# Kernel optimization log

Hardware: AMD Instinct MI355X
Metric: run time of the kernel (lower is better)

Reference implementation:

```python
import jax, jax.numpy as jnp
import numpy as np

DIM = 256
HEADS = 8
DIM_HEAD = 64
SLICE_NUM = 64
INNER = HEADS * DIM_HEAD  # 512
SCALE = DIM_HEAD ** -0.5


def setup_inputs() -> dict:
    key = jax.random.key(0)
    ks = jax.random.split(key, 12)
    b, n = 4, 32768
    s = 0.02
    inp = {
        "x": jax.random.normal(ks[0], (b, n, DIM), dtype=jnp.float32),
        # weights stored as [in, out] so y = x @ W + b
        "W_fx": jax.random.normal(ks[1], (DIM, INNER), dtype=jnp.float32) * s,
        "b_fx": jnp.zeros((INNER,), dtype=jnp.float32),
        "W_x": jax.random.normal(ks[2], (DIM, INNER), dtype=jnp.float32) * s,
        "b_x": jnp.zeros((INNER,), dtype=jnp.float32),
        "W_slice": jax.random.normal(ks[3], (DIM_HEAD, SLICE_NUM), dtype=jnp.float32) * s,
        "b_slice": jnp.zeros((SLICE_NUM,), dtype=jnp.float32),
        "temperature": jnp.ones((1, HEADS, 1, 1), dtype=jnp.float32) * 0.5,
        "Wq": jax.random.normal(ks[4], (DIM_HEAD, DIM_HEAD), dtype=jnp.float32) * s,
        "Wk": jax.random.normal(ks[5], (DIM_HEAD, DIM_HEAD), dtype=jnp.float32) * s,
        "Wv": jax.random.normal(ks[6], (DIM_HEAD, DIM_HEAD), dtype=jnp.float32) * s,
        "W_out": jax.random.normal(ks[7], (INNER, DIM), dtype=jnp.float32) * s,
        "b_out": jnp.zeros((DIM,), dtype=jnp.float32),
    }
    return inp


def reference(x, W_fx, b_fx, W_x, b_x, W_slice, b_slice, temperature,
              Wq, Wk, Wv, W_out, b_out):
    b, n, c = x.shape
    h, d, g = HEADS, DIM_HEAD, SLICE_NUM
    # input projections -> b h n d
    fx_mid = (x @ W_fx + b_fx).reshape(b, n, h, d).transpose(0, 2, 1, 3)
    x_mid = (x @ W_x + b_x).reshape(b, n, h, d).transpose(0, 2, 1, 3)
    # temperature-scaled slice routing softmax: b h n g
    temp = jnp.clip(temperature, 0.1, 5.0)
    slice_logits = (x_mid @ W_slice + b_slice) / temp
    slice_weights = jax.nn.softmax(slice_logits, axis=-1)
    # weighted pooling into slice tokens: b h g d
    slice_tokens = jnp.einsum('bhnc,bhng->bhgc', fx_mid, slice_weights)
    norm = jnp.sum(slice_weights, axis=2)  # b h g
    slice_tokens = slice_tokens / (norm[..., None] + 1e-5)
    # small attention over slice tokens
    q = slice_tokens @ Wq
    k = slice_tokens @ Wk
    v = slice_tokens @ Wv
    attn = jax.nn.softmax(jnp.einsum('bhgd,bhkd->bhgk', q, k) * SCALE, axis=-1)
    out_slice = jnp.einsum('bhgk,bhkd->bhgd', attn, v)
    # scatter back to points: b h n d -> b n (h d)
    out = jnp.einsum('bhgd,bhng->bhnd', out_slice, slice_weights)
    out = out.transpose(0, 2, 1, 3).reshape(b, n, h * d)
    return out @ W_out + b_out
```

## Files before the change

### kernel.cpp

```cpp
#include <hip/hip_runtime.h>
#include <hip/hip_bf16.h>
#include <stdint.h>

#define DIM 256
#define HEADS 8
#define INNER 512
#define NPTS 32768
#define PADN 136
#define PADD 72

typedef unsigned int uint32;
typedef short bf16x8 __attribute__((ext_vector_type(8)));
typedef float f32x4 __attribute__((ext_vector_type(4)));

static __device__ __forceinline__ unsigned short f2bf(float f) {
    unsigned int u = __float_as_uint(f);
    u += 0x7fffu + ((u >> 16) & 1u);
    return (unsigned short)(u >> 16);
}
static __device__ __forceinline__ float bf2f(unsigned short v) {
    return __uint_as_float(((unsigned int)v) << 16);
}
static __device__ __forceinline__ uint32 pkbf(float a, float b) {
    __hip_bfloat162 h = __float22bfloat162_rn(make_float2(a, b));
    return *(reinterpret_cast<uint32*>(&h));
}
static __device__ __forceinline__ void gll16(const void* g, const void* l) {
    __builtin_amdgcn_global_load_lds(
        (const __attribute__((address_space(1))) uint32*)g,
        (__attribute__((address_space(3))) uint32*)l, 16, 0, 0);
}

__global__ __launch_bounds__(256) void k_prep(
    const float* __restrict__ Wfx, const float* __restrict__ Wx,
    const float* __restrict__ Wsl, const float* __restrict__ x,
    unsigned short* __restrict__ Wbt, unsigned short* __restrict__ WslT,
    unsigned short* __restrict__ xb)
{
    const int blk = blockIdx.x, t = threadIdx.x;
    if (blk < 4) {
        const int n = blk * 256 + t;
        for (int k8 = 0; k8 < 256; k8 += 8) {
            unsigned short v[8];
#pragma unroll
            for (int j = 0; j < 8; j++) {
                float f = (n < 512) ? Wfx[(size_t)(k8 + j) * 512 + n]
                                    : Wx[(size_t)(k8 + j) * 512 + (n - 512)];
                v[j] = f2bf(f);
            }
            ushort4 u0 = {v[0], v[1], v[2], v[3]};
            ushort4 u1 = {v[4], v[5], v[6], v[7]};
            *(ushort4*)(Wbt + (size_t)n * 256 + k8) = u0;
            *(ushort4*)(Wbt + (size_t)n * 256 + k8 + 4) = u1;
        }
    } else if (blk == 4) {
        const int g = t >> 2, d0 = (t & 3) * 16;
        unsigned short v[16];
#pragma unroll
        for (int i = 0; i < 16; i++) v[i] = f2bf(Wsl[(size_t)(d0 + i) * 64 + g]);
#pragma unroll
        for (int q = 0; q < 4; q++) {
            ushort4 u = {v[q * 4], v[q * 4 + 1], v[q * 4 + 2], v[q * 4 + 3]};
            *(ushort4*)(WslT + (size_t)g * 64 + d0 + q * 4) = u;
        }
    } else {
        const size_t TOT = (size_t)4 * NPTS * 256;
        size_t i = ((size_t)(blk - 5) * 256 + t) * 8;
        const size_t stride = (size_t)(gridDim.x - 5) * 256 * 8;
        for (; i < TOT; i += stride) {
            float4 f0 = *(const float4*)(x + i);
            float4 f1 = *(const float4*)(x + i + 4);
            uint4 v;
            v.x = pkbf(f0.x, f0.y); v.y = pkbf(f0.z, f0.w);
            v.z = pkbf(f1.x, f1.y); v.w = pkbf(f1.z, f1.w);
            *(uint4*)(xb + i) = v;
        }
    }
}

__global__ __launch_bounds__(256, 3) void k_projfused(
    const unsigned short* __restrict__ xb,
    const unsigned short* __restrict__ Wbt,
    const float* __restrict__ bfx, const float* __restrict__ bx,
    const unsigned short* __restrict__ WslTg,
    const float* __restrict__ bsl, const float* __restrict__ temp,
    unsigned short* __restrict__ wN,
    float* __restrict__ token_num,
    float* __restrict__ norm)
{
    __shared__ unsigned short S[128 * 64 * 2];
    __shared__ unsigned short X[128 * PADD];

    const int L = blockIdx.x;
    const int xcd = L & 7;
    const int j = L >> 3;
    const int chunk = xcd * 32 + (j >> 3);
    const int h = j & 7;

    const int b = chunk >> 6;
    const int t = threadIdx.x;
    const int w = t >> 6, lane = t & 63;
    const int wm = w >> 1, wn = w & 1;
    const int l15 = lane & 15, quad = lane >> 4;

    unsigned short* A  = S;
    unsigned short* Bs = S + 128 * 64;
    unsigned short* fxS = S;
    unsigned short* wsmT = X;

    bf16x8 wslf[4][2];
#pragma unroll
    for (int c = 0; c < 4; c++)
#pragma unroll
        for (int ks = 0; ks < 2; ks++)
            wslf[c][ks] = *(const bf16x8*)&WslTg[(c * 16 + l15) * 64 + ks * 32 + quad * 8];

    float tv = temp[h];
    tv = fminf(fmaxf(tv, 0.1f), 5.0f);
    const float itemp = 1.0f / tv;
    float bsl_c[4], bfx_c[4], bx_c[4];
#pragma unroll
    for (int c = 0; c < 4; c++) {
        bsl_c[c] = bsl[c * 16 + l15];
        bfx_c[c] = bfx[h * 64 + c * 16 + l15];
        bx_c[c]  = bx[h * 64 + c * 16 + l15];
    }

    f32x4 pacc[4];
#pragma unroll
    for (int c = 0; c < 4; c++) pacc[c] = (f32x4){0.f, 0.f, 0.f, 0.f};
    float ns[4] = {0.f, 0.f, 0.f, 0.f};

    for (int mt = 0; mt < 4; mt++) {
        const int n_in_b = ((chunk & 63) * 4 + mt) * 128;
        const size_t m0 = (size_t)b * NPTS + n_in_b;

        f32x4 acc[4][4];
#pragma unroll
        for (int r = 0; r < 4; r++)
#pragma unroll
            for (int c = 0; c < 4; c++) acc[r][c] = (f32x4){0.f, 0.f, 0.f, 0.f};

        for (int kb = 0; kb < 256; kb += 64) {
            __syncthreads();
#pragma unroll
            for (int rr = 0; rr < 4; rr++) {
                int flat = rr * 256 + t;
                int row = flat >> 3, colg = (flat & 7) * 8;
                gll16(xb + (m0 + row) * 256 + kb + colg, (char*)A + flat * 16);
                int grow = (rr < 2) ? (h * 64 + row) : (512 + h * 64 + (row - 64));
                gll16(Wbt + (size_t)grow * 256 + kb + colg, (char*)Bs + flat * 16);
            }
            __syncthreads();
#pragma unroll
            for (int ks = 0; ks < 2; ks++) {
                bf16x8 af[4], bfv[4];
#pragma unroll
                for (int r = 0; r < 4; r++)
                    af[r] = *(const bf16x8*)&A[(wm * 64 + r * 16 + l15) * 64 + ks * 32 + quad * 8];
#pragma unroll
                for (int c = 0; c < 4; c++)
                    bfv[c] = *(const bf16x8*)&Bs[(wn * 64 + c * 16 + l15) * 64 + ks * 32 + quad * 8];
#pragma unroll
                for (int r = 0; r < 4; r++)
#pragma unroll
                    for (int c = 0; c < 4; c++)
                        acc[r][c] = __builtin_amdgcn_mfma_f32_16x16x32_bf16(af[r], bfv[c], acc[r][c], 0, 0, 0);
            }
        }

        __syncthreads();
        if (wn == 0) {
#pragma unroll
            for (int r = 0; r < 4; r++)
#pragma unroll
                for (int c = 0; c < 4; c++) {
                    ushort4 u;
                    u.x = f2bf(acc[r][c][0] + bfx_c[c]);
                    u.y = f2bf(acc[r][c][1] + bfx_c[c]);
                    u.z = f2bf(acc[r][c][2] + bfx_c[c]);
                    u.w = f2bf(acc[r][c][3] + bfx_c[c]);
                    *(ushort4*)&fxS[(c * 16 + l15) * PADN + wm * 64 + r * 16 + quad * 4] = u;
                }
        } else {
#pragma unroll
            for (int r = 0; r < 4; r++)
#pragma unroll
                for (int c = 0; c < 4; c++)
#pragma unroll
                    for (int j2 = 0; j2 < 4; j2++)
                        X[(wm * 64 + r * 16 + quad * 4 + j2) * PADD + c * 16 + l15] =
                            f2bf(acc[r][c][j2] + bx_c[c]);
        }
        __syncthreads();

        f32x4 lacc[2][4];
#pragma unroll
        for (int rt = 0; rt < 2; rt++)
#pragma unroll
            for (int c = 0; c < 4; c++)
                lacc[rt][c] = (f32x4){bsl_c[c], bsl_c[c], bsl_c[c], bsl_c[c]};
#pragma unroll
        for (int ks = 0; ks < 2; ks++) {
            bf16x8 laf[2];
#pragma unroll
            for (int rt = 0; rt < 2; rt++)
                laf[rt] = *(const bf16x8*)&X[(w * 32 + rt * 16 + l15) * PADD + ks * 32 + quad * 8];
#pragma unroll
            for (int rt = 0; rt < 2; rt++)
#pragma unroll
                for (int c = 0; c < 4; c++)
                    lacc[rt][c] = __builtin_amdgcn_mfma_f32_16x16x32_bf16(laf[rt], wslf[c][ks], lacc[rt][c], 0, 0, 0);
        }
        __syncthreads();

#pragma unroll
        for (int rt = 0; rt < 2; rt++) {
            float wv[4][4];
#pragma unroll
            for (int j2 = 0; j2 < 4; j2++) {
                float v0 = lacc[rt][0][j2] * itemp;
                float v1 = lacc[rt][1][j2] * itemp;
                float v2 = lacc[rt][2][j2] * itemp;
                float v3 = lacc[rt][3][j2] * itemp;
                float mx = fmaxf(fmaxf(v0, v1), fmaxf(v2, v3));
                mx = fmaxf(mx, __shfl_xor(mx, 1));
                mx = fmaxf(mx, __shfl_xor(mx, 2));
                mx = fmaxf(mx, __shfl_xor(mx, 4));
                mx = fmaxf(mx, __shfl_xor(mx, 8));
                float e0 = __expf(v0 - mx), e1 = __expf(v1 - mx);
                float e2 = __expf(v2 - mx), e3 = __expf(v3 - mx);
                float s = e0 + e1 + e2 + e3;
                s += __shfl_xor(s, 1);
                s += __shfl_xor(s, 2);
                s += __shfl_xor(s, 4);
                s += __shfl_xor(s, 8);
                float inv = 1.0f / s;
                wv[0][j2] = e0 * inv; wv[1][j2] = e1 * inv;
                wv[2][j2] = e2 * inv; wv[3][j2] = e3 * inv;
                ns[0] += wv[0][j2]; ns[1] += wv[1][j2];
                ns[2] += wv[2][j2]; ns[3] += wv[3][j2];
            }
#pragma unroll
            for (int c = 0; c < 4; c++) {
                ushort4 u;
                u.x = f2bf(wv[c][0]); u.y = f2bf(wv[c][1]);
                u.z = f2bf(wv[c][2]); u.w = f2bf(wv[c][3]);
                *(ushort4*)&wsmT[(c * 16 + l15) * PADN + w * 32 + rt * 16 + quad * 4] = u;
            }
        }
        __syncthreads();

#pragma unroll
        for (int kk = 0; kk < 4; kk++) {
            bf16x8 paf = *(const bf16x8*)&wsmT[(w * 16 + l15) * PADN + kk * 32 + quad * 8];
#pragma unroll
            for (int c = 0; c < 4; c++) {
                bf16x8 pbf = *(const bf16x8*)&fxS[(c * 16 + l15) * PADN + kk * 32 + quad * 8];
                pacc[c] = __builtin_amdgcn_mfma_f32_16x16x32_bf16(paf, pbf, pacc[c], 0, 0, 0);
            }
        }

        {
            const int n = t >> 1, half = t & 1;
            unsigned short* dst = wN + ((size_t)b * NPTS + n_in_b + n) * 512 + h * 64 + half * 32;
#pragma unroll
            for (int g8 = 0; g8 < 4; g8++) {
                unsigned short tmp[8];
#pragma unroll
                for (int i = 0; i < 8; i++)
                    tmp[i] = wsmT[(half * 32 + g8 * 8 + i) * PADN + n];
                *(uint4*)(dst + g8 * 8) = *(const uint4*)tmp;
            }
        }
    }

    float* tn = token_num + ((size_t)(b * 8 + h) * 64) * 64;
#pragma unroll
    for (int c = 0; c < 4; c++)
#pragma unroll
        for (int j2 = 0; j2 < 4; j2++)
            atomicAdd(tn + (size_t)(w * 16 + quad * 4 + j2) * 64 + c * 16 + l15, pacc[c][j2]);
#pragma unroll
    for (int c = 0; c < 4; c++) {
        ns[c] += __shfl_xor(ns[c], 16);
        ns[c] += __shfl_xor(ns[c], 32);
    }
    if (quad == 0) {
#pragma unroll
        for (int c = 0; c < 4; c++)
            atomicAdd(norm + ((size_t)b * 8 + h) * 64 + c * 16 + l15, ns[c]);
    }
}

__global__ __launch_bounds__(256) void k_attn(
    const float* __restrict__ token_num, const float* __restrict__ norm,
    const float* __restrict__ Wq, const float* __restrict__ Wk,
    const float* __restrict__ Wv, float* __restrict__ out_slice)
{
    const int bh = blockIdx.x;
    const int t = threadIdx.x;
    const int gg = t >> 2, qq = t & 3;

    __shared__ float tok[64][68];
    __shared__ float qS[64][68];
    __shared__ float kS[64][68];
    __shared__ float vS[64][68];
    __shared__ float pS[64][68];
    __shared__ float Wqs[64][64], Wks[64][64], Wvs[64][64];

    for (int i = t; i < 4096; i += 256) {
        int g = i >> 6, dd = i & 63;
        Wqs[g][dd] = Wq[i];
        Wks[g][dd] = Wk[i];
        Wvs[g][dd] = Wv[i];
        tok[g][dd] = token_num[(size_t)bh * 4096 + i] / (norm[bh * 64 + g] + 1e-5f);
    }
    __syncthreads();

    float aq[16] = {}, ak[16] = {}, av[16] = {};
    for (int k = 0; k < 64; k++) {
        const float tv = tok[gg][k];
        const float4* wq4 = (const float4*)&Wqs[k][qq * 16];
        const float4* wk4 = (const float4*)&Wks[k][qq * 16];
        const float4* wv4 = (const float4*)&Wvs[k][qq * 16];
#pragma unroll
        for (int j4 = 0; j4 < 4; j4++) {
            float4 a = wq4[j4], bq = wk4[j4], c = wv4[j4];
            aq[j4*4+0] = fmaf(tv, a.x,  aq[j4*4+0]);
            aq[j4*4+1] = fmaf(tv, a.y,  aq[j4*4+1]);
            aq[j4*4+2] = fmaf(tv, a.z,  aq[j4*4+2]);
            aq[j4*4+3] = fmaf(tv, a.w,  aq[j4*4+3]);
            ak[j4*4+0] = fmaf(tv, bq.x, ak[j4*4+0]);
            ak[j4*4+1] = fmaf(tv, bq.y, ak[j4*4+1]);
            ak[j4*4+2] = fmaf(tv, bq.z, ak[j4*4+2]);
            ak[j4*4+3] = fmaf(tv, bq.w, ak[j4*4+3]);
            av[j4*4+0] = fmaf(tv, c.x,  av[j4*4+0]);
            av[j4*4+1] = fmaf(tv, c.y,  av[j4*4+1]);
            av[j4*4+2] = fmaf(tv, c.z,  av[j4*4+2]);
            av[j4*4+3] = fmaf(tv, c.w,  av[j4*4+3]);
        }
    }
#pragma unroll
    for (int j = 0; j < 16; j++) {
        qS[gg][qq * 16 + j] = aq[j];
        kS[gg][qq * 16 + j] = ak[j];
        vS[gg][qq * 16 + j] = av[j];
    }
    __syncthreads();

    float sc[16] = {};
    for (int d4 = 0; d4 < 16; d4++) {
        float4 q4 = *(const float4*)&qS[gg][d4 * 4];
#pragma unroll
        for (int j = 0; j < 16; j++) {
            float4 k4 = *(const float4*)&kS[qq * 16 + j][d4 * 4];
            sc[j] = fmaf(q4.x, k4.x, sc[j]);
            sc[j] = fmaf(q4.y, k4.y, sc[j]);
            sc[j] = fmaf(q4.z, k4.z, sc[j]);
            sc[j] = fmaf(q4.w, k4.w, sc[j]);
        }
    }
    const float SCALE = 0.125f;
    float mx = -1e30f;
#pragma unroll
    for (int j = 0; j < 16; j++) { sc[j] *= SCALE; mx = fmaxf(mx, sc[j]); }
    mx = fmaxf(mx, __shfl_xor(mx, 1));
    mx = fmaxf(mx, __shfl_xor(mx, 2));
    float s = 0.f;
#pragma unroll
    for (int j = 0; j < 16; j++) { sc[j] = __expf(sc[j] - mx); s += sc[j]; }
    s += __shfl_xor(s, 1);
    s += __shfl_xor(s, 2);
    const float invs = 1.0f / s;
#pragma unroll
    for (int j = 0; j < 16; j++) pS[gg][qq * 16 + j] = sc[j] * invs;
    __syncthreads();

    float oo[16] = {};
    for (int j = 0; j < 64; j++) {
        const float pv = pS[gg][j];
        const float4* v4p = (const float4*)&vS[j][qq * 16];
#pragma unroll
        for (int d4 = 0; d4 < 4; d4++) {
            float4 v4 = v4p[d4];
            oo[d4*4+0] = fmaf(pv, v4.x, oo[d4*4+0]);
            oo[d4*4+1] = fmaf(pv, v4.y, oo[d4*4+1]);
            oo[d4*4+2] = fmaf(pv, v4.z, oo[d4*4+2]);
            oo[d4*4+3] = fmaf(pv, v4.w, oo[d4*4+3]);
        }
    }
    float* op = out_slice + (size_t)bh * 4096 + gg * 64 + qq * 16;
#pragma unroll
    for (int d4 = 0; d4 < 4; d4++) {
        float4 o; o.x = oo[d4*4+0]; o.y = oo[d4*4+1]; o.z = oo[d4*4+2]; o.w = oo[d4*4+3];
        *(float4*)(op + d4 * 4) = o;
    }
}

__global__ __launch_bounds__(256) void k_m(
    const float* __restrict__ os, const float* __restrict__ W_out,
    unsigned short* __restrict__ Mt_hi, unsigned short* __restrict__ Mt_lo)
{
    const int h = blockIdx.x, b = blockIdx.y;
    const int t = threadIdx.x;
    __shared__ float osl[64][65];
    for (int i = t; i < 4096; i += 256)
        osl[i >> 6][i & 63] = os[(size_t)(b * 8 + h) * 4096 + i];
    __syncthreads();
    float acc[64];
#pragma unroll
    for (int g = 0; g < 64; g++) acc[g] = 0.f;
    for (int d = 0; d < 64; d++) {
        float wv = W_out[(size_t)(h * 64 + d) * 256 + t];
#pragma unroll
        for (int g = 0; g < 64; g++) acc[g] = fmaf(osl[g][d], wv, acc[g]);
    }
    unsigned short* ph = Mt_hi + (size_t)(b * 256 + t) * 512 + h * 64;
    unsigned short* pl = Mt_lo + (size_t)(b * 256 + t) * 512 + h * 64;
#pragma unroll
    for (int g4 = 0; g4 < 16; g4++) {
        ushort4 uh, ul;
        unsigned short hh; float v, lo;
        v = acc[g4*4+0]; hh = f2bf(v); lo = v - bf2f(hh); uh.x = hh; ul.x = f2bf(lo);
        v = acc[g4*4+1]; hh = f2bf(v); lo = v - bf2f(hh); uh.y = hh; ul.y = f2bf(lo);
        v = acc[g4*4+2]; hh = f2bf(v); lo = v - bf2f(hh); uh.z = hh; ul.z = f2bf(lo);
        v = acc[g4*4+3]; hh = f2bf(v); lo = v - bf2f(hh); uh.w = hh; ul.w = f2bf(lo);
        *(ushort4*)(ph + g4 * 4) = uh;
        *(ushort4*)(pl + g4 * 4) = ul;
    }
}

__global__ __launch_bounds__(256, 3) void k_out(
    const unsigned short* __restrict__ wN,
    const unsigned short* __restrict__ Mt_hi, const unsigned short* __restrict__ Mt_lo,
    const float* __restrict__ bout, float* __restrict__ out)
{
    __shared__ unsigned short A[128 * 64];
    __shared__ unsigned short Bh[128 * 64];
    __shared__ unsigned short Bl[128 * 64];
    const int L = blockIdx.x;
    const int xcd = L & 7;
    const int j = L >> 3;
    const int mtile = xcd * 128 + (j >> 1);
    const int ntile = j & 1;
    const int m0 = mtile * 128, col0 = ntile * 128;
    const int b = m0 >> 15;
    const int t = threadIdx.x;
    const int w = t >> 6, lane = t & 63, l15 = lane & 15, quad = lane >> 4;
    const int wm = w >> 1, wn = w & 1;

    f32x4 acc[4][4];
#pragma unroll
    for (int r = 0; r < 4; r++)
#pragma unroll
        for (int c = 0; c < 4; c++) acc[r][c] = (f32x4){0.f, 0.f, 0.f, 0.f};

    for (int kb = 0; kb < 512; kb += 64) {
        __syncthreads();
#pragma unroll
        for (int rr = 0; rr < 4; rr++) {
            int flat = rr * 256 + t;
            int row = flat >> 3, col = (flat & 7) * 8;
            gll16(wN + (size_t)(m0 + row) * 512 + kb + col, (char*)A + flat * 16);
            gll16(Mt_hi + (size_t)(b * 256 + col0 + row) * 512 + kb + col, (char*)Bh + flat * 16);
            gll16(Mt_lo + (size_t)(b * 256 + col0 + row) * 512 + kb + col, (char*)Bl + flat * 16);
        }
        __syncthreads();
#pragma unroll
        for (int ks = 0; ks < 2; ks++) {
            bf16x8 af[4], bh4[4], bl4[4];
#pragma unroll
            for (int r = 0; r < 4; r++)
                af[r] = *(const bf16x8*)&A[(wm * 64 + r * 16 + l15) * 64 + ks * 32 + quad * 8];
#pragma unroll
            for (int c = 0; c < 4; c++) {
                bh4[c] = *(const bf16x8*)&Bh[(wn * 64 + c * 16 + l15) * 64 + ks * 32 + quad * 8];
                bl4[c] = *(const bf16x8*)&Bl[(wn * 64 + c * 16 + l15) * 64 + ks * 32 + quad * 8];
            }
#pragma unroll
            for (int r = 0; r < 4; r++)
#pragma unroll
                for (int c = 0; c < 4; c++) {
                    acc[r][c] = __builtin_amdgcn_mfma_f32_16x16x32_bf16(af[r], bh4[c], acc[r][c], 0, 0, 0);
                    acc[r][c] = __builtin_amdgcn_mfma_f32_16x16x32_bf16(af[r], bl4[c], acc[r][c], 0, 0, 0);
                }
        }
    }
    float biasc[4];
#pragma unroll
    for (int c = 0; c < 4; c++) biasc[c] = bout[col0 + wn * 64 + c * 16 + l15];
#pragma unroll
    for (int r = 0; r < 4; r++)
#pragma unroll
        for (int c = 0; c < 4; c++)
#pragma unroll
            for (int j2 = 0; j2 < 4; j2++)
                out[(size_t)(m0 + wm * 64 + r * 16 + quad * 4 + j2) * 256 + col0 + wn * 64 + c * 16 + l15] =
                    acc[r][c][j2] + biasc[c];
}

extern "C" void kernel_launch(void* const* d_in, const int* in_sizes, int n_in,
                              void* d_out, int out_size, void* d_ws, size_t ws_size,
                              hipStream_t stream) {
    const float* x    = (const float*)d_in[0];
    const float* Wfx  = (const float*)d_in[1];
    const float* bfx  = (const float*)d_in[2];
    const float* Wx   = (const float*)d_in[3];
    const float* bx   = (const float*)d_in[4];
    const float* Wsl  = (const float*)d_in[5];
    const float* bsl  = (const float*)d_in[6];
    const float* temp = (const float*)d_in[7];
    const float* Wq   = (const float*)d_in[8];
    const float* Wk   = (const float*)d_in[9];
    const float* Wv   = (const float*)d_in[10];
    const float* Wout = (const float*)d_in[11];
    const float* bout = (const float*)d_in[12];
    float* out = (float*)d_out;

    const int Mtotal = in_sizes[0] / DIM;
    const int B = Mtotal / NPTS;

    char* p = (char*)d_ws;
    unsigned short* Wbt   = (unsigned short*)p; p += (size_t)1024 * 256 * 2;
    unsigned short* WslTg = (unsigned short*)p; p += (size_t)64 * 64 * 2;
    unsigned short* wN    = (unsigned short*)p; p += (size_t)Mtotal * INNER * 2;
    float* token_num = (float*)p; p += (size_t)B * 8 * 64 * 64 * 4;
    float* norm_ws   = (float*)p; p += (size_t)B * 8 * 64 * 4;
    float* os_ws     = (float*)p; p += (size_t)B * 8 * 64 * 64 * 4;
    unsigned short* Mt_hi = (unsigned short*)p; p += (size_t)B * 256 * 512 * 2;
    unsigned short* Mt_lo = (unsigned short*)p; p += (size_t)B * 256 * 512 * 2;

    unsigned short* xb = (unsigned short*)d_out;

    hipMemsetAsync(token_num, 0,
                   (size_t)B * 8 * 64 * 64 * 4 + (size_t)B * 8 * 64 * 4, stream);

    k_prep<<<2048, 256, 0, stream>>>(Wfx, Wx, Wsl, x, Wbt, WslTg, xb);
    k_projfused<<<2048, 256, 0, stream>>>(
        xb, Wbt, bfx, bx, WslTg, bsl, temp, wN, token_num, norm_ws);
    k_attn<<<B * 8, 256, 0, stream>>>(token_num, norm_ws, Wq, Wk, Wv, os_ws);
    k_m<<<dim3(8, B), 256, 0, stream>>>(os_ws, Wout, Mt_hi, Mt_lo);
    k_out<<<2048, 256, 0, stream>>>(wN, Mt_hi, Mt_lo, bout, out);
}
```

Baseline: 784.0 us.

## Replace global atomics with per-chunk partial buffers and a separate reduction kernel

The fused projection kernel no longer atomically accumulates slice-token sums and norms into shared global arrays. Each block now writes its partial tile with nontemporal stores into a scratch area placed in the output buffer, and a new reduction kernel sums the 64 chunk partials per batch-head. This also removes the memset of the accumulators and makes the wN stores nontemporal. The cost is an extra kernel launch plus roughly 32 MB of extra partial-buffer writes and reads.

```diff
diff --git a/kernel.cpp b/kernel.cpp
--- a/kernel.cpp
+++ b/kernel.cpp
@@ -12,6 +12,7 @@
 typedef unsigned int uint32;
 typedef short bf16x8 __attribute__((ext_vector_type(8)));
 typedef float f32x4 __attribute__((ext_vector_type(4)));
+typedef uint32 u32x4 __attribute__((ext_vector_type(4)));
 
 static __device__ __forceinline__ unsigned short f2bf(float f) {
     unsigned int u = __float_as_uint(f);
@@ -29,6 +30,9 @@
     __builtin_amdgcn_global_load_lds(
         (const __attribute__((address_space(1))) uint32*)g,
         (__attribute__((address_space(3))) uint32*)l, 16, 0, 0);
+}
+static __device__ __forceinline__ void nts16(const void* src, void* dst) {
+    __builtin_nontemporal_store(*(const u32x4*)src, (u32x4*)dst);
 }
 
 __global__ __launch_bounds__(256) void k_prep(
@@ -70,10 +74,10 @@
         for (; i < TOT; i += stride) {
             float4 f0 = *(const float4*)(x + i);
             float4 f1 = *(const float4*)(x + i + 4);
-            uint4 v;
+            u32x4 v;
             v.x = pkbf(f0.x, f0.y); v.y = pkbf(f0.z, f0.w);
             v.z = pkbf(f1.x, f1.y); v.w = pkbf(f1.z, f1.w);
-            *(uint4*)(xb + i) = v;
+            *(u32x4*)(xb + i) = v;
         }
     }
 }
@@ -85,8 +89,8 @@
     const unsigned short* __restrict__ WslTg,
     const float* __restrict__ bsl, const float* __restrict__ temp,
     unsigned short* __restrict__ wN,
-    float* __restrict__ token_num,
-    float* __restrict__ norm)
+    float* __restrict__ tp,
+    float* __restrict__ np)
 {
     __shared__ unsigned short S[128 * 64 * 2];
     __shared__ unsigned short X[128 * PADD];
@@ -270,26 +274,47 @@
 #pragma unroll
                 for (int i = 0; i < 8; i++)
                     tmp[i] = wsmT[(half * 32 + g8 * 8 + i) * PADN + n];
-                *(uint4*)(dst + g8 * 8) = *(const uint4*)tmp;
-            }
-        }
-    }
-
-    float* tn = token_num + ((size_t)(b * 8 + h) * 64) * 64;
+                nts16(tmp, dst + g8 * 8);
+            }
+        }
+    }
+
+    const size_t cb = (size_t)(b * 8 + h) * 64 + (chunk & 63);
+    float* tpb = tp + cb * 4096;
 #pragma unroll
     for (int c = 0; c < 4; c++)
 #pragma unroll
         for (int j2 = 0; j2 < 4; j2++)
-            atomicAdd(tn + (size_t)(w * 16 + quad * 4 + j2) * 64 + c * 16 + l15, pacc[c][j2]);
+            __builtin_nontemporal_store(pacc[c][j2],
+                tpb + (size_t)(w * 16 + quad * 4 + j2) * 64 + c * 16 + l15);
 #pragma unroll
     for (int c = 0; c < 4; c++) {
         ns[c] += __shfl_xor(ns[c], 16);
         ns[c] += __shfl_xor(ns[c], 32);
     }
     if (quad == 0) {
+        float* npb = np + (cb * 4 + w) * 64;
 #pragma unroll
         for (int c = 0; c < 4; c++)
-            atomicAdd(norm + ((size_t)b * 8 + h) * 64 + c * 16 + l15, ns[c]);
+            __builtin_nontemporal_store(ns[c], npb + c * 16 + l15);
+    }
+}
+
+__global__ __launch_bounds__(256) void k_red(
+    const float* __restrict__ tp, const float* __restrict__ np,
+    float* __restrict__ token_num, float* __restrict__ norm)
+{
+    const int bh = blockIdx.x >> 4, seg = blockIdx.x & 15;
+    const int t = threadIdx.x;
+    float s = 0.f;
+    const float* base = tp + (size_t)bh * 64 * 4096 + seg * 256 + t;
+    for (int c = 0; c < 64; c++) s += base[(size_t)c * 4096];
+    token_num[(size_t)bh * 4096 + seg * 256 + t] = s;
+    if (seg == 0 && t < 64) {
+        float nsum = 0.f;
+        const float* nb = np + (size_t)bh * 64 * 4 * 64 + t;
+        for (int i = 0; i < 256; i++) nsum += nb[(size_t)i * 64];
+        norm[bh * 64 + t] = nsum;
     }
 }
 
@@ -532,13 +557,13 @@
     unsigned short* Mt_lo = (unsigned short*)p; p += (size_t)B * 256 * 512 * 2;
 
     unsigned short* xb = (unsigned short*)d_out;
-
-    hipMemsetAsync(token_num, 0,
-                   (size_t)B * 8 * 64 * 64 * 4 + (size_t)B * 8 * 64 * 4, stream);
+    float* tp = (float*)((char*)d_out + (size_t)Mtotal * DIM * 2);
+    float* np = tp + (size_t)B * 8 * 64 * 4096;
 
     k_prep<<<2048, 256, 0, stream>>>(Wfx, Wx, Wsl, x, Wbt, WslTg, xb);
     k_projfused<<<2048, 256, 0, stream>>>(
-        xb, Wbt, bfx, bx, WslTg, bsl, temp, wN, token_num, norm_ws);
+        xb, Wbt, bfx, bx, WslTg, bsl, temp, wN, tp, np);
+    k_red<<<B * 8 * 16, 256, 0, stream>>>(tp, np, token_num, norm_ws);
     k_attn<<<B * 8, 256, 0, stream>>>(token_num, norm_ws, Wq, Wk, Wv, os_ws);
     k_m<<<dim3(8, B), 256, 0, stream>>>(os_ws, Wout, Mt_hi, Mt_lo);
     k_out<<<2048, 256, 0, stream>>>(wN, Mt_hi, Mt_lo, bout, out);
```

New measurement: 813.0 us. 3.7% more time.
